# Performance work log

Measured on AMD Instinct MI355X. Metric: run time of the kernel, lower is better.

Reference implementation:

```python
import jax, jax.numpy as jnp
import numpy as np

DT_MIN, DT_MAX = 0.001, 0.1
CHUNK = 64


def setup_inputs() -> dict:
    key = jax.random.key(0)
    ks = jax.random.split(key, 8)
    b, L, D = 2, 4096, 1024
    d_inner, d_state, nheads, K = 2048, 128, 32, 4
    conv_dim = d_inner + 2 * d_state            # 2304
    d_in_proj = 2 * d_inner + 2 * d_state + nheads  # 4384
    f32 = jnp.float32
    return {
        'x': jax.random.normal(ks[0], (b, L, D), f32),
        'in_proj_w': jax.random.normal(ks[1], (d_in_proj, D), f32) * (D ** -0.5),
        'conv_w': jax.random.normal(ks[2], (conv_dim, K), f32) * 0.3,
        'conv_b': jnp.zeros((conv_dim,), f32),
        'dt_bias': jax.random.normal(ks[3], (nheads,), f32) * 0.5,
        'A_log': jnp.log(jax.random.uniform(ks[4], (nheads,), f32, 1.0, 16.0)),
        'D_skip': jnp.ones((nheads,), f32),
        'norm_w': jnp.ones((d_inner,), f32),
        'out_proj_w': jax.random.normal(ks[5], (D, d_inner), f32) * (d_inner ** -0.5),
        'ln_w': jnp.ones((D,), f32),
        'ln_b': jnp.zeros((D,), f32),
    }


def reference(x, in_proj_w, conv_w, conv_b, dt_bias, A_log, D_skip, norm_w, out_proj_w, ln_w, ln_b):
    b, L, d_model = x.shape
    d_inner = norm_w.shape[0]
    nheads = A_log.shape[0]
    hd = d_inner // nheads                      # headdim = 64
    conv_dim = conv_w.shape[0]
    d_state = (conv_dim - d_inner) // 2
    Q = CHUNK
    c = L // Q

    # ---- Mamba2 in_proj ----
    zxbcdt = jnp.einsum('bld,kd->blk', x, in_proj_w)
    z = zxbcdt[..., :d_inner]                                   # gate
    xBC = zxbcdt[..., d_inner:d_inner + conv_dim]
    dt_raw = zxbcdt[..., d_inner + conv_dim:]                   # (b,L,h)

    # ---- causal depthwise conv1d (kernel 4) + SiLU ----
    K = conv_w.shape[1]
    xp = jnp.pad(xBC, ((0, 0), (K - 1, 0), (0, 0)))
    conv = sum(xp[:, k:k + L, :] * conv_w[:, k] for k in range(K)) + conv_b
    xBC = jax.nn.silu(conv)
    x_ssm = xBC[..., :d_inner]
    Bm = xBC[..., d_inner:d_inner + d_state]                    # (b,L,n)
    Cm = xBC[..., d_inner + d_state:]                           # (b,L,n)

    # ---- bounded dt (sigmoid, per SSMBlock fix) ----
    dt = DT_MIN + (DT_MAX - DT_MIN) * jax.nn.sigmoid(dt_raw + dt_bias)  # (b,L,h)
    A = -jnp.exp(A_log)                                          # (h,)

    # ---- chunked SSD selective scan ----
    xh = x_ssm.reshape(b, c, Q, nheads, hd)
    dtc = dt.reshape(b, c, Q, nheads)
    x_dt = xh * dtc[..., None]
    dA = jnp.einsum('bcqh,h->bhcq', dtc, A)
    Acum = jnp.cumsum(dA, axis=-1)                               # (b,h,c,Q)
    Bc = Bm.reshape(b, c, Q, d_state)
    Cc = Cm.reshape(b, c, Q, d_state)

    # intra-chunk (diagonal blocks)
    seg = Acum[..., :, None] - Acum[..., None, :]                # (b,h,c,Q,Q)
    mask = jnp.tril(jnp.ones((Q, Q), bool))
    Lmat = jnp.exp(jnp.where(mask, seg, -jnp.inf))
    Yd = jnp.einsum('bcqn,bcsn,bhcqs,bcshp->bcqhp', Cc, Bc, Lmat, x_dt)

    # chunk end-states
    decay_states = jnp.exp(Acum[..., -1:] - Acum)                # (b,h,c,Q)
    states = jnp.einsum('bcqn,bhcq,bcqhp->bchpn', Bc, decay_states, x_dt)
    chunk_decay = jnp.exp(Acum[..., -1])                         # (b,h,c)

    def step(carry, inp):
        st, dec = inp
        return dec[..., None, None] * carry + st, carry

    _, prevs = jax.lax.scan(
        step, jnp.zeros((b, nheads, hd, d_state), x.dtype),
        (jnp.moveaxis(states, 1, 0), jnp.moveaxis(chunk_decay, 2, 0)))
    prevs = jnp.moveaxis(prevs, 0, 1)                            # (b,c,h,p,n)

    # inter-chunk contribution
    Yo = jnp.einsum('bcqn,bchpn,bhcq->bcqhp', Cc, prevs, jnp.exp(Acum))

    Y = (Yd + Yo).reshape(b, L, nheads, hd) + D_skip[None, None, :, None] * xh.reshape(b, L, nheads, hd)
    y = Y.reshape(b, L, d_inner)

    # ---- gated RMSNorm + out_proj ----
    y = y * jax.nn.silu(z)
    y = y * jax.lax.rsqrt(jnp.mean(y * y, axis=-1, keepdims=True) + 1e-5) * norm_w
    out = jnp.einsum('bli,di->bld', y, out_proj_w)

    # ---- SSMBlock: LayerNorm + (eval-mode dropout) + residual ----
    mu = jnp.mean(out, axis=-1, keepdims=True)
    var = jnp.mean((out - mu) ** 2, axis=-1, keepdims=True)
    ln = (out - mu) * jax.lax.rsqrt(var + 1e-5) * ln_w + ln_b
    return x + ln
```

## Files before the change

### kernel.cpp

```cpp
#include <hip/hip_runtime.h>
#include <math.h>

#define BSZ     2
#define LEN     4096
#define DMODEL  1024
#define DINNER  2048
#define DSTATE  128
#define NHEADS  32
#define HDIM    64
#define CONVDIM 2304
#define QC      64
#define NCHUNK  64
#define ROWS    (BSZ*LEN)
#define SDIM    (HDIM*DSTATE)
#define PB      136
#define PT      72
#define CGRP    (CONVDIM/8)

typedef __attribute__((ext_vector_type(8))) short short8;
typedef __attribute__((ext_vector_type(4))) float f32x4;

__device__ __forceinline__ float silu_(float x){ return x / (1.0f + expf(-x)); }
__device__ __forceinline__ float sigm_(float x){ return 1.0f / (1.0f + expf(-x)); }
__device__ __forceinline__ float bf2f(unsigned short u){
    return __uint_as_float(((unsigned int)u) << 16);
}
__device__ __forceinline__ unsigned short f2bf(float f){
    unsigned int u = __float_as_uint(f);
    u = (u + 0x7fffu + ((u >> 16) & 1u)) >> 16;
    return (unsigned short)u;
}

__device__ __forceinline__ void gload16(const void* g, void* l) {
    __builtin_amdgcn_global_load_lds(
        (const __attribute__((address_space(1))) unsigned int*)g,
        (__attribute__((address_space(3))) unsigned int*)l, 16, 0, 0);
}

__global__ __launch_bounds__(256) void cast_bf16(const float* __restrict__ src,
                                                 unsigned short* __restrict__ dst,
                                                 int n4) {
    const int i = blockIdx.x * 256 + threadIdx.x;
    if (i >= n4) return;
    const float4 v = *(const float4*)(src + (size_t)i * 4);
    ushort4 o;
    o.x = f2bf(v.x); o.y = f2bf(v.y); o.z = f2bf(v.z); o.w = f2bf(v.w);
    *(ushort4*)(dst + (size_t)i * 4) = o;
}

template<bool BF16OUT>
__global__ __launch_bounds__(256) void gemm_bt_mfma(const unsigned short* __restrict__ A,
                                                    const unsigned short* __restrict__ B,
                                                    void* __restrict__ Cout,
                                                    int N, int K) {
    __shared__ unsigned short As[128 * 32];
    __shared__ unsigned short Bs[128 * 32];
    const int tid = threadIdx.x;
    const int wave = tid >> 6, lane = tid & 63;
    const int m0 = blockIdx.y * 128, n0 = blockIdx.x * 128;
    const int m_off = (wave >> 1) * 64, n_off = (wave & 1) * 64;

    f32x4 acc[4][4];
#pragma unroll
    for (int i = 0; i < 4; i++)
#pragma unroll
        for (int j = 0; j < 4; j++) acc[i][j] = (f32x4){0.f, 0.f, 0.f, 0.f};

    const int arow = m_off + (lane & 15);
    const int brow = n_off + (lane & 15);
    const int koff = (lane >> 4) * 16;

    for (int kt = 0; kt < K; kt += 32) {
#pragma unroll
        for (int u = 0; u < 2; u++) {
            const int f = u * 256 + tid;
            const int row = f >> 2;
            const int ke = (f & 3) * 8;
            gload16(A + (size_t)(m0 + row) * K + kt + ke, ((char*)As) + f * 16);
            gload16(B + (size_t)(n0 + row) * K + kt + ke, ((char*)Bs) + f * 16);
        }
        __syncthreads();
        short8 af[4], bfr[4];
#pragma unroll
        for (int i = 0; i < 4; i++)
            af[i] = *(const short8*)((const char*)As + (arow + i * 16) * 64 + koff);
#pragma unroll
        for (int j = 0; j < 4; j++)
            bfr[j] = *(const short8*)((const char*)Bs + (brow + j * 16) * 64 + koff);
#pragma unroll
        for (int i = 0; i < 4; i++)
#pragma unroll
            for (int j = 0; j < 4; j++)
                acc[i][j] = __builtin_amdgcn_mfma_f32_16x16x32_bf16(
                    af[i], bfr[j], acc[i][j], 0, 0, 0);
        __syncthreads();
    }

    const int crow = (lane >> 4) * 4;
    const int ccol = lane & 15;
#pragma unroll
    for (int i = 0; i < 4; i++)
#pragma unroll
        for (int j = 0; j < 4; j++) {
            const int n = n0 + n_off + j * 16 + ccol;
#pragma unroll
            for (int r = 0; r < 4; r++) {
                const int m = m0 + m_off + i * 16 + crow + r;
                if (BF16OUT)
                    ((unsigned short*)Cout)[(size_t)m * N + n] = f2bf(acc[i][j][r]);
                else
                    ((float*)Cout)[(size_t)m * N + n] = acc[i][j][r];
            }
        }
}

__global__ __launch_bounds__(256) void dtproj_mfma(const unsigned short* __restrict__ A,
                                                   const unsigned short* __restrict__ W,
                                                   const float* __restrict__ bias,
                                                   float* __restrict__ dtb,
                                                   int K) {
    __shared__ unsigned short As[128 * 32];
    __shared__ unsigned short Bs[32 * 32];
    const int tid = threadIdx.x;
    const int wave = tid >> 6, lane = tid & 63;
    const int quad = lane >> 4, l16 = lane & 15;
    const int m0 = blockIdx.x * 128;

    f32x4 acc[2][2];
#pragma unroll
    for (int i = 0; i < 2; i++)
#pragma unroll
        for (int j = 0; j < 2; j++) acc[i][j] = (f32x4){0.f, 0.f, 0.f, 0.f};

    for (int kt = 0; kt < K; kt += 32) {
#pragma unroll
        for (int u = 0; u < 2; u++) {
            const int f = u * 256 + tid;
            const int row = f >> 2, ke = (f & 3) * 8;
            gload16(A + (size_t)(m0 + row) * K + kt + ke, ((char*)As) + f * 16);
        }
        if (tid < 128) {
            const int row = tid >> 2, ke = (tid & 3) * 8;
            gload16(W + (size_t)row * K + kt + ke, ((char*)Bs) + tid * 16);
        }
        __syncthreads();
        short8 af[2], bfr[2];
#pragma unroll
        for (int i = 0; i < 2; i++)
            af[i] = *(const short8*)((const char*)As + (wave * 32 + i * 16 + l16) * 64 + quad * 16);
#pragma unroll
        for (int j = 0; j < 2; j++)
            bfr[j] = *(const short8*)((const char*)Bs + (j * 16 + l16) * 64 + quad * 16);
#pragma unroll
        for (int i = 0; i < 2; i++)
#pragma unroll
            for (int j = 0; j < 2; j++)
                acc[i][j] = __builtin_amdgcn_mfma_f32_16x16x32_bf16(
                    af[i], bfr[j], acc[i][j], 0, 0, 0);
        __syncthreads();
    }
#pragma unroll
    for (int i = 0; i < 2; i++)
#pragma unroll
        for (int j = 0; j < 2; j++) {
            const int h = j * 16 + l16;
            const float bh = bias[h];
#pragma unroll
            for (int r = 0; r < 4; r++) {
                const int m = m0 + wave * 32 + i * 16 + quad * 4 + r;
                dtb[(size_t)m * NHEADS + h] =
                    0.001f + 0.099f * sigm_(acc[i][j][r] + bh);
            }
        }
}

__global__ __launch_bounds__(256) void conv_silu_w(const unsigned short* __restrict__ xbc,
                                                   const float* __restrict__ cw,
                                                   const float* __restrict__ cb,
                                                   unsigned short* __restrict__ xssm,
                                                   unsigned short* __restrict__ Bb,
                                                   unsigned short* __restrict__ Cb) {
    const int idx = blockIdx.x * 256 + threadIdx.x;
    const int g = idx % CGRP;
    const int rowblk = idx / CGRP;
    const long row0 = (long)rowblk * 4;
    const int lbase = (int)(row0 & (LEN - 1));
    const int j0 = g * 8;

    float4 wv[8];
    float cbv[8];
#pragma unroll
    for (int e = 0; e < 8; e++) {
        wv[e] = *(const float4*)(cw + (size_t)(j0 + e) * 4);
        cbv[e] = cb[j0 + e];
    }

    short8 win[4];
    const short8 zero8 = (short8){0, 0, 0, 0, 0, 0, 0, 0};
#pragma unroll
    for (int t = 0; t < 3; t++) {
        const int lr = lbase - 3 + t;
        win[t] = (lr >= 0) ? *(const short8*)(xbc + (row0 - 3 + t) * CONVDIM + j0)
                           : zero8;
    }
#pragma unroll
    for (int i = 0; i < 4; i++) {
        win[3] = *(const short8*)(xbc + (row0 + i) * CONVDIM + j0);
        short8 o;
#pragma unroll
        for (int e = 0; e < 8; e++) {
            float acc = cbv[e];
            acc += bf2f((unsigned short)win[0][e]) * wv[e].x;
            acc += bf2f((unsigned short)win[1][e]) * wv[e].y;
            acc += bf2f((unsigned short)win[2][e]) * wv[e].z;
            acc += bf2f((unsigned short)win[3][e]) * wv[e].w;
            o[e] = (short)f2bf(silu_(acc));
        }
        const long row = row0 + i;
        if (j0 < DINNER)
            *(short8*)(xssm + row * DINNER + j0) = o;
        else if (j0 < DINNER + DSTATE)
            *(short8*)(Bb + row * DSTATE + (j0 - DINNER)) = o;
        else
            *(short8*)(Cb + row * DSTATE + (j0 - DINNER - DSTATE)) = o;
        win[0] = win[1]; win[1] = win[2]; win[2] = win[3];
    }
}

__global__ __launch_bounds__(64) void acum_kernel(const float* __restrict__ dtb,
                                                  const float* __restrict__ A_log,
                                                  float* __restrict__ Acum) {
    const int c = blockIdx.x, h = blockIdx.y, b = blockIdx.z;
    const int q = threadIdx.x;
    const float Av = -expf(A_log[h]);
    float v = dtb[((size_t)b * LEN + c * QC + q) * NHEADS + h] * Av;
#pragma unroll
    for (int off = 1; off < 64; off <<= 1) {
        const float n = __shfl_up(v, off, 64);
        if (q >= off) v += n;
    }
    Acum[(((size_t)b * NHEADS + h) * NCHUNK + c) * QC + q] = v;
}

__global__ __launch_bounds__(256) void chunk_mfma(const unsigned short* __restrict__ xssm,
                                                  const unsigned short* __restrict__ Bb,
                                                  const unsigned short* __restrict__ Cb,
                                                  const float* __restrict__ dtb,
                                                  const float* __restrict__ Acum,
                                                  const float* __restrict__ Dskip,
                                                  unsigned short* __restrict__ Y,
                                                  unsigned short* __restrict__ states) {
    const int c = blockIdx.x, h = blockIdx.y, b = blockIdx.z;
    const int tid = threadIdx.x;
    const int wave = tid >> 6, lane = tid & 63;
    const int quad = lane >> 4, l16 = lane & 15;

    __shared__ __attribute__((aligned(16))) unsigned short Bsh[8704];
    __shared__ __attribute__((aligned(16))) unsigned short Csh[9216];
    __shared__ __attribute__((aligned(16))) unsigned short xTs[4608];
    __shared__ float ac[QC], dts[QC], decs[QC];

    const size_t rowbase = (size_t)b * LEN + c * QC;
    if (tid < QC) {
        ac[tid]  = Acum[(((size_t)b * NHEADS + h) * NCHUNK + c) * QC + tid];
        dts[tid] = dtb[(rowbase + tid) * NHEADS + h];
    }
#pragma unroll
    for (int u = 0; u < 4; u++) {
        const int vi = u * 256 + tid;
        const int s = vi >> 4, n0 = (vi & 15) * 8;
        *(short8*)&Bsh[s * PB + n0] = *(const short8*)(Bb + (rowbase + s) * DSTATE + n0);
        *(short8*)&Csh[s * PB + n0] = *(const short8*)(Cb + (rowbase + s) * DSTATE + n0);
    }
#pragma unroll
    for (int u = 0; u < 2; u++) {
        const int vi = u * 256 + tid;
        const int q = vi >> 3, p0 = (vi & 7) * 8;
        const short8 v = *(const short8*)(xssm + (rowbase + q) * DINNER + h * HDIM + p0);
#pragma unroll
        for (int j = 0; j < 8; j++) xTs[(p0 + j) * PT + q] = (unsigned short)v[j];
    }
    __syncthreads();
    if (tid < QC) decs[tid] = expf(ac[QC - 1] - ac[tid]) * dts[tid];

    f32x4 S[4];
#pragma unroll
    for (int j = 0; j < 4; j++) S[j] = (f32x4){0.f, 0.f, 0.f, 0.f};
    const int qa = wave * 16 + l16;
#pragma unroll
    for (int ks = 0; ks < 4; ks++) {
        const short8 a = *(const short8*)&Csh[qa * PB + ks * 32 + quad * 8];
#pragma unroll
        for (int j = 0; j < 4; j++) {
            const short8 bb = *(const short8*)&Bsh[(j * 16 + l16) * PB + ks * 32 + quad * 8];
            S[j] = __builtin_amdgcn_mfma_f32_16x16x32_bf16(a, bb, S[j], 0, 0, 0);
        }
    }
    unsigned short slv[4][4];
#pragma unroll
    for (int j = 0; j < 4; j++)
#pragma unroll
        for (int r = 0; r < 4; r++) {
            const int q = wave * 16 + quad * 4 + r, s = j * 16 + l16;
            const float v = (s <= q) ? S[j][r] * expf(ac[q] - ac[s]) * dts[s] : 0.f;
            slv[j][r] = f2bf(v);
        }
    __syncthreads();

#pragma unroll
    for (int u = 0; u < 4; u++) {
        const int vi = u * 256 + tid;
        const int s = vi >> 4, n0 = (vi & 15) * 8;
        const short8 v = *(const short8*)&Bsh[s * PB + n0];
        const float d = decs[s];
#pragma unroll
        for (int j = 0; j < 8; j++)
            Csh[(n0 + j) * PT + s] = f2bf(bf2f((unsigned short)v[j]) * d);
    }
    __syncthreads();

#pragma unroll
    for (int j = 0; j < 4; j++)
#pragma unroll
        for (int r = 0; r < 4; r++)
            Bsh[(wave * 16 + quad * 4 + r) * PT + j * 16 + l16] = slv[j][r];
    __syncthreads();

    f32x4 yd[4];
#pragma unroll
    for (int j = 0; j < 4; j++) yd[j] = (f32x4){0.f, 0.f, 0.f, 0.f};
#pragma unroll
    for (int ks = 0; ks < 2; ks++) {
        const short8 a = *(const short8*)&Bsh[qa * PT + ks * 32 + quad * 8];
#pragma unroll
        for (int j = 0; j < 4; j++) {
            const short8 xb = *(const short8*)&xTs[(j * 16 + l16) * PT + ks * 32 + quad * 8];
            yd[j] = __builtin_amdgcn_mfma_f32_16x16x32_bf16(a, xb, yd[j], 0, 0, 0);
        }
    }
    const float Dh = Dskip[h];
#pragma unroll
    for (int j = 0; j < 4; j++)
#pragma unroll
        for (int r = 0; r < 4; r++) {
            const int q = wave * 16 + quad * 4 + r, p = j * 16 + l16;
            const float v = yd[j][r] + Dh * bf2f(xTs[p * PT + q]);
            Y[(rowbase + q) * DINNER + h * HDIM + p] = f2bf(v);
        }

    f32x4 st[8];
#pragma unroll
    for (int j = 0; j < 8; j++) st[j] = (f32x4){0.f, 0.f, 0.f, 0.f};
#pragma unroll
    for (int ks = 0; ks < 2; ks++) {
        const short8 a = *(const short8*)&xTs[qa * PT + ks * 32 + quad * 8];
#pragma unroll
        for (int j = 0; j < 8; j++) {
            const short8 bb = *(const short8*)&Csh[(j * 16 + l16) * PT + ks * 32 + quad * 8];
            st[j] = __builtin_amdgcn_mfma_f32_16x16x32_bf16(a, bb, st[j], 0, 0, 0);
        }
    }
    const size_t sbase = (((size_t)b * NHEADS + h) * NCHUNK + c) * SDIM;
#pragma unroll
    for (int j = 0; j < 8; j++)
#pragma unroll
        for (int r = 0; r < 4; r++) {
            const int p = wave * 16 + quad * 4 + r, n = j * 16 + l16;
            states[sbase + (size_t)p * DSTATE + n] = f2bf(st[j][r]);
        }
}

__global__ __launch_bounds__(256) void scan_kernel(unsigned short* __restrict__ states,
                                                   const float* __restrict__ Acum) {
    __shared__ float dec[NCHUNK];
    const int bh = blockIdx.y;
    const int pn = blockIdx.x * 256 + threadIdx.x;
    if (threadIdx.x < NCHUNK)
        dec[threadIdx.x] = expf(Acum[((size_t)bh * NCHUNK + threadIdx.x) * QC + (QC - 1)]);
    __syncthreads();
    float carry = 0.f;
    const size_t base = (size_t)bh * NCHUNK * SDIM + pn;
    for (int c = 0; c < NCHUNK; c++) {
        const size_t idx = base + (size_t)c * SDIM;
        const float s = bf2f(states[idx]);
        states[idx] = f2bf(carry);
        carry = dec[c] * carry + s;
    }
}

__global__ __launch_bounds__(256) void yo_mfma(const unsigned short* __restrict__ Cb,
                                               const unsigned short* __restrict__ prevs,
                                               const float* __restrict__ Acum,
                                               unsigned short* __restrict__ Y) {
    const int c = blockIdx.x, h = blockIdx.y, b = blockIdx.z;
    const int tid = threadIdx.x;
    const int wave = tid >> 6, lane = tid & 63;
    const int quad = lane >> 4, l16 = lane & 15;
    __shared__ __attribute__((aligned(16))) unsigned short Csh[8704];
    __shared__ __attribute__((aligned(16))) unsigned short Psh[8704];
    __shared__ float eq[QC];
    const size_t rowbase = (size_t)b * LEN + c * QC;
    const size_t pbase = (((size_t)b * NHEADS + h) * NCHUNK + c) * SDIM;
    if (tid < QC)
        eq[tid] = expf(Acum[(((size_t)b * NHEADS + h) * NCHUNK + c) * QC + tid]);
#pragma unroll
    for (int u = 0; u < 4; u++) {
        const int vi = u * 256 + tid;
        const int r = vi >> 4, n0 = (vi & 15) * 8;
        *(short8*)&Csh[r * PB + n0] = *(const short8*)(Cb + (rowbase + r) * DSTATE + n0);
        *(short8*)&Psh[r * PB + n0] = *(const short8*)(prevs + pbase + (size_t)r * DSTATE + n0);
    }
    __syncthreads();

    f32x4 acc[4];
#pragma unroll
    for (int j = 0; j < 4; j++) acc[j] = (f32x4){0.f, 0.f, 0.f, 0.f};
    const int qa = wave * 16 + l16;
#pragma unroll
    for (int ks = 0; ks < 4; ks++) {
        const short8 a = *(const short8*)&Csh[qa * PB + ks * 32 + quad * 8];
#pragma unroll
        for (int j = 0; j < 4; j++) {
            const short8 bb = *(const short8*)&Psh[(j * 16 + l16) * PB + ks * 32 + quad * 8];
            acc[j] = __builtin_amdgcn_mfma_f32_16x16x32_bf16(a, bb, acc[j], 0, 0, 0);
        }
    }
#pragma unroll
    for (int j = 0; j < 4; j++)
#pragma unroll
        for (int r = 0; r < 4; r++) {
            const int q = wave * 16 + quad * 4 + r, p = j * 16 + l16;
            const size_t off = (rowbase + q) * DINNER + h * HDIM + p;
            Y[off] = f2bf(bf2f(Y[off]) + eq[q] * acc[j][r]);
        }
}

__global__ __launch_bounds__(256) void gate_rms(const unsigned short* __restrict__ Y,
                                                const unsigned short* __restrict__ zbf,
                                                const float* __restrict__ nw,
                                                unsigned short* __restrict__ ybf) {
    const int r = blockIdx.x, tid = threadIdx.x;
    float4 yv[2];
    float ss = 0.f;
#pragma unroll
    for (int u = 0; u < 2; u++) {
        const int col = u * 1024 + tid * 4;
        const ushort4 y4 = *(const ushort4*)(Y + (size_t)r * DINNER + col);
        const ushort4 z4 = *(const ushort4*)(zbf + (size_t)r * DINNER + col);
        float4 y;
        y.x = bf2f(y4.x) * silu_(bf2f(z4.x)); y.y = bf2f(y4.y) * silu_(bf2f(z4.y));
        y.z = bf2f(y4.z) * silu_(bf2f(z4.z)); y.w = bf2f(y4.w) * silu_(bf2f(z4.w));
        yv[u] = y;
        ss += y.x * y.x + y.y * y.y + y.z * y.z + y.w * y.w;
    }
#pragma unroll
    for (int off = 32; off; off >>= 1) ss += __shfl_xor(ss, off, 64);
    __shared__ float red[4];
    if ((tid & 63) == 0) red[tid >> 6] = ss;
    __syncthreads();
    ss = red[0] + red[1] + red[2] + red[3];
    const float scale = rsqrtf(ss / (float)DINNER + 1e-5f);
#pragma unroll
    for (int u = 0; u < 2; u++) {
        const int col = u * 1024 + tid * 4;
        const float4 w4 = *(const float4*)(nw + col);
        ushort4 o;
        o.x = f2bf(yv[u].x * scale * w4.x); o.y = f2bf(yv[u].y * scale * w4.y);
        o.z = f2bf(yv[u].z * scale * w4.z); o.w = f2bf(yv[u].w * scale * w4.w);
        *(ushort4*)(ybf + (size_t)r * DINNER + col) = o;
    }
}

__global__ __launch_bounds__(256) void ln_res(const float* __restrict__ outb,
                                              const float* __restrict__ x,
                                              const float* __restrict__ lw,
                                              const float* __restrict__ lb,
                                              float* __restrict__ out) {
    const int r = blockIdx.x, tid = threadIdx.x;
    const int col = tid * 4;
    const float4 v = *(const float4*)(outb + (size_t)r * DMODEL + col);
    float s = v.x + v.y + v.z + v.w;
    float s2 = v.x * v.x + v.y * v.y + v.z * v.z + v.w * v.w;
#pragma unroll
    for (int off = 32; off; off >>= 1) {
        s += __shfl_xor(s, off, 64);
        s2 += __shfl_xor(s2, off, 64);
    }
    __shared__ float rs[4], rs2[4];
    if ((tid & 63) == 0) { rs[tid >> 6] = s; rs2[tid >> 6] = s2; }
    __syncthreads();
    s = rs[0] + rs[1] + rs[2] + rs[3];
    s2 = rs2[0] + rs2[1] + rs2[2] + rs2[3];
    const float mu = s / (float)DMODEL;
    const float var = s2 / (float)DMODEL - mu * mu;
    const float inv = rsqrtf(var + 1e-5f);
    const float4 xw = *(const float4*)(x + (size_t)r * DMODEL + col);
    const float4 w4 = *(const float4*)(lw + col);
    const float4 b4 = *(const float4*)(lb + col);
    float4 o;
    o.x = xw.x + (v.x - mu) * inv * w4.x + b4.x;
    o.y = xw.y + (v.y - mu) * inv * w4.y + b4.y;
    o.z = xw.z + (v.z - mu) * inv * w4.z + b4.z;
    o.w = xw.w + (v.w - mu) * inv * w4.w + b4.w;
    *(float4*)(out + (size_t)r * DMODEL + col) = o;
}

extern "C" void kernel_launch(void* const* d_in, const int* in_sizes, int n_in,
                              void* d_out, int out_size, void* d_ws, size_t ws_size,
                              hipStream_t stream) {
    const float* x          = (const float*)d_in[0];
    const float* in_proj_w  = (const float*)d_in[1];
    const float* conv_w     = (const float*)d_in[2];
    const float* conv_b     = (const float*)d_in[3];
    const float* dt_bias    = (const float*)d_in[4];
    const float* A_log      = (const float*)d_in[5];
    const float* D_skip     = (const float*)d_in[6];
    const float* norm_w     = (const float*)d_in[7];
    const float* out_proj_w = (const float*)d_in[8];
    const float* ln_w       = (const float*)d_in[9];
    const float* ln_b       = (const float*)d_in[10];
    float* out = (float*)d_out;
    float* ws = (float*)d_ws;

    size_t off = 0;
    unsigned short* zbf     = (unsigned short*)(ws + off); off += (size_t)ROWS * DINNER / 2;
    unsigned short* xssm_bf = (unsigned short*)(ws + off); off += (size_t)ROWS * DINNER / 2;
    unsigned short* uni     = (unsigned short*)(ws + off); off += (size_t)ROWS * CONVDIM / 2;
    unsigned short* Bb_bf   = (unsigned short*)(ws + off); off += (size_t)ROWS * DSTATE / 2;
    unsigned short* Cb_bf   = (unsigned short*)(ws + off); off += (size_t)ROWS * DSTATE / 2;
    float* dtb   = ws + off; off += (size_t)ROWS * NHEADS;
    float* Acum  = ws + off; off += (size_t)BSZ * NHEADS * NCHUNK * QC;
    unsigned short* x_bf  = (unsigned short*)(ws + off); off += (size_t)ROWS * DMODEL / 2;
    unsigned short* wi_bf = (unsigned short*)(ws + off); off += (size_t)4384 * DMODEL / 2;
    unsigned short* wo_bf = (unsigned short*)(ws + off); off += (size_t)DMODEL * DINNER / 2;
    unsigned short* states = (unsigned short*)(ws + off); off += (size_t)BSZ * NHEADS * NCHUNK * SDIM / 2;
    const size_t need_bytes = off * sizeof(float);
    if (ws_size < need_bytes) return;

    unsigned short* xbc_bf = uni;
    unsigned short* Ybf    = uni;
    unsigned short* ybf    = xssm_bf;

    cast_bf16<<<(ROWS * DMODEL / 4 + 255) / 256, 256, 0, stream>>>(x, x_bf, ROWS * DMODEL / 4);
    cast_bf16<<<(4384 * DMODEL / 4 + 255) / 256, 256, 0, stream>>>(in_proj_w, wi_bf, 4384 * DMODEL / 4);
    cast_bf16<<<(DMODEL * DINNER / 4 + 255) / 256, 256, 0, stream>>>(out_proj_w, wo_bf, DMODEL * DINNER / 4);

    gemm_bt_mfma<true><<<dim3(DINNER / 128, ROWS / 128), 256, 0, stream>>>(
        x_bf, wi_bf, zbf, DINNER, DMODEL);
    gemm_bt_mfma<true><<<dim3(CONVDIM / 128, ROWS / 128), 256, 0, stream>>>(
        x_bf, wi_bf + (size_t)DINNER * DMODEL, xbc_bf, CONVDIM, DMODEL);
    dtproj_mfma<<<ROWS / 128, 256, 0, stream>>>(
        x_bf, wi_bf + (size_t)(DINNER + CONVDIM) * DMODEL, dt_bias, dtb, DMODEL);

    conv_silu_w<<<(ROWS / 4) * CGRP / 256, 256, 0, stream>>>(
        xbc_bf, conv_w, conv_b, xssm_bf, Bb_bf, Cb_bf);
    acum_kernel<<<dim3(NCHUNK, NHEADS, BSZ), 64, 0, stream>>>(dtb, A_log, Acum);
    chunk_mfma<<<dim3(NCHUNK, NHEADS, BSZ), 256, 0, stream>>>(
        xssm_bf, Bb_bf, Cb_bf, dtb, Acum, D_skip, Ybf, states);
    scan_kernel<<<dim3(SDIM / 256, BSZ * NHEADS), 256, 0, stream>>>(states, Acum);
    yo_mfma<<<dim3(NCHUNK, NHEADS, BSZ), 256, 0, stream>>>(Cb_bf, states, Acum, Ybf);
    gate_rms<<<ROWS, 256, 0, stream>>>(Ybf, zbf, norm_w, ybf);

    gemm_bt_mfma<false><<<dim3(DMODEL / 128, ROWS / 128), 256, 0, stream>>>(
        ybf, wo_bf, out, DMODEL, DINNER);
    ln_res<<<ROWS, 256, 0, stream>>>(out, x, ln_w, ln_b, out);
}
```

Before: 475.4 us.

## Swizzle chunk LDS tiles and read B/C MFMA operands directly from global

Replaces the padded shared-memory tiles in chunk_mfma with XOR-swizzled 64-wide layouts for xT, the scaled B-transpose and the masked score matrix. It also drops the shared staging of B and C, loading MFMA operands straight from global memory, and computes the decay factor inline. That removes one barrier and shrinks LDS use. In yo_mfma, C is likewise read directly from global instead of through LDS. The aim is fewer LDS bank conflicts, fewer syncs and higher occupancy, at the cost of repeated uncoalesced global reads of B and C.

```diff
diff --git a/kernel.cpp b/kernel.cpp
--- a/kernel.cpp
+++ b/kernel.cpp
@@ -14,7 +14,6 @@
 #define ROWS    (BSZ*LEN)
 #define SDIM    (HDIM*DSTATE)
 #define PB      136
-#define PT      72
 #define CGRP    (CONVDIM/8)
 
 typedef __attribute__((ext_vector_type(8))) short short8;
@@ -29,6 +28,13 @@
     unsigned int u = __float_as_uint(f);
     u = (u + 0x7fffu + ((u >> 16) & 1u)) >> 16;
     return (unsigned short)u;
+}
+
+__device__ __forceinline__ int sw_el(int r, int c) {
+    return r * 64 + ((((c >> 3) ^ (r & 7) ^ ((r >> 3) & 7)) << 3) | (c & 7));
+}
+__device__ __forceinline__ int sw_blk(int r, int bl) {
+    return r * 64 + (((bl ^ (r & 7) ^ ((r >> 3) & 7)) << 3));
 }
 
 __device__ __forceinline__ void gload16(const void* g, void* l) {
@@ -255,86 +261,73 @@
     const int wave = tid >> 6, lane = tid & 63;
     const int quad = lane >> 4, l16 = lane & 15;
 
-    __shared__ __attribute__((aligned(16))) unsigned short Bsh[8704];
-    __shared__ __attribute__((aligned(16))) unsigned short Csh[9216];
-    __shared__ __attribute__((aligned(16))) unsigned short xTs[4608];
-    __shared__ float ac[QC], dts[QC], decs[QC];
+    __shared__ __attribute__((aligned(16))) unsigned short xTs[64 * 64];
+    __shared__ __attribute__((aligned(16))) unsigned short Bp[128 * 64];
+    __shared__ __attribute__((aligned(16))) unsigned short SLs[64 * 64];
+    __shared__ float ac[QC], dts[QC];
 
     const size_t rowbase = (size_t)b * LEN + c * QC;
     if (tid < QC) {
         ac[tid]  = Acum[(((size_t)b * NHEADS + h) * NCHUNK + c) * QC + tid];
         dts[tid] = dtb[(rowbase + tid) * NHEADS + h];
     }
-#pragma unroll
-    for (int u = 0; u < 4; u++) {
-        const int vi = u * 256 + tid;
-        const int s = vi >> 4, n0 = (vi & 15) * 8;
-        *(short8*)&Bsh[s * PB + n0] = *(const short8*)(Bb + (rowbase + s) * DSTATE + n0);
-        *(short8*)&Csh[s * PB + n0] = *(const short8*)(Cb + (rowbase + s) * DSTATE + n0);
-    }
+
 #pragma unroll
     for (int u = 0; u < 2; u++) {
         const int vi = u * 256 + tid;
         const int q = vi >> 3, p0 = (vi & 7) * 8;
         const short8 v = *(const short8*)(xssm + (rowbase + q) * DINNER + h * HDIM + p0);
 #pragma unroll
-        for (int j = 0; j < 8; j++) xTs[(p0 + j) * PT + q] = (unsigned short)v[j];
+        for (int j = 0; j < 8; j++)
+            xTs[sw_el(p0 + j, q)] = (unsigned short)v[j];
+    }
+
+    const int qa = wave * 16 + l16;
+    f32x4 S[4];
+#pragma unroll
+    for (int j = 0; j < 4; j++) S[j] = (f32x4){0.f, 0.f, 0.f, 0.f};
+#pragma unroll
+    for (int ks = 0; ks < 4; ks++) {
+        const short8 a = *(const short8*)(Cb + (rowbase + qa) * DSTATE + ks * 32 + quad * 8);
+#pragma unroll
+        for (int j = 0; j < 4; j++) {
+            const short8 bb = *(const short8*)(Bb + (rowbase + j * 16 + l16) * DSTATE + ks * 32 + quad * 8);
+            S[j] = __builtin_amdgcn_mfma_f32_16x16x32_bf16(a, bb, S[j], 0, 0, 0);
+        }
     }
     __syncthreads();
-    if (tid < QC) decs[tid] = expf(ac[QC - 1] - ac[tid]) * dts[tid];
-
-    f32x4 S[4];
-#pragma unroll
-    for (int j = 0; j < 4; j++) S[j] = (f32x4){0.f, 0.f, 0.f, 0.f};
-    const int qa = wave * 16 + l16;
-#pragma unroll
-    for (int ks = 0; ks < 4; ks++) {
-        const short8 a = *(const short8*)&Csh[qa * PB + ks * 32 + quad * 8];
-#pragma unroll
-        for (int j = 0; j < 4; j++) {
-            const short8 bb = *(const short8*)&Bsh[(j * 16 + l16) * PB + ks * 32 + quad * 8];
-            S[j] = __builtin_amdgcn_mfma_f32_16x16x32_bf16(a, bb, S[j], 0, 0, 0);
-        }
-    }
-    unsigned short slv[4][4];
+
+    const float ac63 = ac[QC - 1];
 #pragma unroll
     for (int j = 0; j < 4; j++)
 #pragma unroll
         for (int r = 0; r < 4; r++) {
             const int q = wave * 16 + quad * 4 + r, s = j * 16 + l16;
             const float v = (s <= q) ? S[j][r] * expf(ac[q] - ac[s]) * dts[s] : 0.f;
-            slv[j][r] = f2bf(v);
-        }
-    __syncthreads();
-
+            SLs[sw_el(q, s)] = f2bf(v);
+        }
 #pragma unroll
     for (int u = 0; u < 4; u++) {
         const int vi = u * 256 + tid;
         const int s = vi >> 4, n0 = (vi & 15) * 8;
-        const short8 v = *(const short8*)&Bsh[s * PB + n0];
-        const float d = decs[s];
+        const short8 v = *(const short8*)(Bb + (rowbase + s) * DSTATE + n0);
+        const float d = expf(ac63 - ac[s]) * dts[s];
 #pragma unroll
         for (int j = 0; j < 8; j++)
-            Csh[(n0 + j) * PT + s] = f2bf(bf2f((unsigned short)v[j]) * d);
+            Bp[sw_el(n0 + j, s)] = f2bf(bf2f((unsigned short)v[j]) * d);
     }
     __syncthreads();
 
-#pragma unroll
-    for (int j = 0; j < 4; j++)
-#pragma unroll
-        for (int r = 0; r < 4; r++)
-            Bsh[(wave * 16 + quad * 4 + r) * PT + j * 16 + l16] = slv[j][r];
-    __syncthreads();
-
     f32x4 yd[4];
 #pragma unroll
     for (int j = 0; j < 4; j++) yd[j] = (f32x4){0.f, 0.f, 0.f, 0.f};
 #pragma unroll
     for (int ks = 0; ks < 2; ks++) {
-        const short8 a = *(const short8*)&Bsh[qa * PT + ks * 32 + quad * 8];
+        const short8 a = *(const short8*)&SLs[sw_blk(qa, ks * 4 + quad)];
 #pragma unroll
         for (int j = 0; j < 4; j++) {
-            const short8 xb = *(const short8*)&xTs[(j * 16 + l16) * PT + ks * 32 + quad * 8];
+            const int p = j * 16 + l16;
+            const short8 xb = *(const short8*)&xTs[sw_blk(p, ks * 4 + quad)];
             yd[j] = __builtin_amdgcn_mfma_f32_16x16x32_bf16(a, xb, yd[j], 0, 0, 0);
         }
     }
@@ -344,7 +337,7 @@
 #pragma unroll
         for (int r = 0; r < 4; r++) {
             const int q = wave * 16 + quad * 4 + r, p = j * 16 + l16;
-            const float v = yd[j][r] + Dh * bf2f(xTs[p * PT + q]);
+            const float v = yd[j][r] + Dh * bf2f(xTs[sw_el(p, q)]);
             Y[(rowbase + q) * DINNER + h * HDIM + p] = f2bf(v);
         }
 
@@ -353,10 +346,11 @@
     for (int j = 0; j < 8; j++) st[j] = (f32x4){0.f, 0.f, 0.f, 0.f};
 #pragma unroll
     for (int ks = 0; ks < 2; ks++) {
-        const short8 a = *(const short8*)&xTs[qa * PT + ks * 32 + quad * 8];
+        const short8 a = *(const short8*)&xTs[sw_blk(qa, ks * 4 + quad)];
 #pragma unroll
         for (int j = 0; j < 8; j++) {
-            const short8 bb = *(const short8*)&Csh[(j * 16 + l16) * PT + ks * 32 + quad * 8];
+            const int n = j * 16 + l16;
+            const short8 bb = *(const short8*)&Bp[sw_blk(n, ks * 4 + quad)];
             st[j] = __builtin_amdgcn_mfma_f32_16x16x32_bf16(a, bb, st[j], 0, 0, 0);
         }
     }
@@ -396,7 +390,6 @@
     const int tid = threadIdx.x;
     const int wave = tid >> 6, lane = tid & 63;
     const int quad = lane >> 4, l16 = lane & 15;
-    __shared__ __attribute__((aligned(16))) unsigned short Csh[8704];
     __shared__ __attribute__((aligned(16))) unsigned short Psh[8704];
     __shared__ float eq[QC];
     const size_t rowbase = (size_t)b * LEN + c * QC;
@@ -407,7 +400,6 @@
     for (int u = 0; u < 4; u++) {
         const int vi = u * 256 + tid;
         const int r = vi >> 4, n0 = (vi & 15) * 8;
-        *(short8*)&Csh[r * PB + n0] = *(const short8*)(Cb + (rowbase + r) * DSTATE + n0);
         *(short8*)&Psh[r * PB + n0] = *(const short8*)(prevs + pbase + (size_t)r * DSTATE + n0);
     }
     __syncthreads();
@@ -418,7 +410,7 @@
     const int qa = wave * 16 + l16;
 #pragma unroll
     for (int ks = 0; ks < 4; ks++) {
-        const short8 a = *(const short8*)&Csh[qa * PB + ks * 32 + quad * 8];
+        const short8 a = *(const short8*)(Cb + (rowbase + qa) * DSTATE + ks * 32 + quad * 8);
 #pragma unroll
         for (int j = 0; j < 4; j++) {
             const short8 bb = *(const short8*)&Psh[(j * 16 + l16) * PB + ks * 32 + quad * 8];
```

Result: slower. 485.9 us (+2.2%).
